# Kernel tuning notes

Hardware: AMD Instinct MI355X
Metric: run time of the kernel (lower is better)

## Reference

```python
import jax, jax.numpy as jnp
import numpy as np

D_MODEL = 2048
N_HEADS = 16
D_HEAD = 128
INIT_RANGE = 0.02
EPSILON = -100000.0  # mask fill value from the original module


def setup_inputs() -> dict:
    key = jax.random.key(0)
    ks = jax.random.split(key, 6)
    x = jax.random.normal(ks[0], (2, 2048, D_MODEL), dtype=jnp.float32)
    W_Q = jax.random.normal(ks[1], (N_HEADS, D_MODEL, D_HEAD), dtype=jnp.float32) * INIT_RANGE
    W_K = jax.random.normal(ks[2], (N_HEADS, D_MODEL, D_HEAD), dtype=jnp.float32) * INIT_RANGE
    W_V = jax.random.normal(ks[3], (N_HEADS, D_MODEL, D_HEAD), dtype=jnp.float32) * INIT_RANGE
    W_O = jax.random.normal(ks[4], (N_HEADS, D_HEAD, D_MODEL), dtype=jnp.float32) * INIT_RANGE
    b_Q = jnp.zeros((N_HEADS, D_HEAD), dtype=jnp.float32)
    b_K = jnp.zeros((N_HEADS, D_HEAD), dtype=jnp.float32)
    b_V = jnp.zeros((N_HEADS, D_HEAD), dtype=jnp.float32)
    b_O = jnp.zeros((D_MODEL,), dtype=jnp.float32)
    return {"normalized_resid_pre": x, "W_Q": W_Q, "b_Q": b_Q, "W_K": W_K,
            "b_K": b_K, "W_V": W_V, "b_V": b_V, "W_O": W_O, "b_O": b_O}


def reference(normalized_resid_pre, W_Q, b_Q, W_K, b_K, W_V, b_V, W_O, b_O):
    x = normalized_resid_pre  # [b, s, d_model]
    # per-head projections: [b, s, h, d_head]
    q = jnp.einsum('bsd,hdk->bshk', x, W_Q) + b_Q
    k = jnp.einsum('bsd,hdk->bshk', x, W_K) + b_K
    v = jnp.einsum('bsd,hdk->bshk', x, W_V) + b_V
    # attention scores [b, h, q, k]
    scores = jnp.einsum('bqhk,bshk->bhqs', q, k) / jnp.sqrt(jnp.float32(D_HEAD))
    S = scores.shape[-1]
    causal = jnp.tril(jnp.ones((S, S), dtype=bool))  # True = keep
    scores = jnp.where(causal, scores, jnp.float32(EPSILON))
    pattern = jax.nn.softmax(scores, axis=-1)
    z = jnp.einsum('bhqs,bshk->bqhk', pattern, v)
    attn_out = jnp.einsum('bqhk,hkd->bqd', z, W_O) + b_O
    return attn_out
```

## Files before the change

### kernel.cpp

```cpp
#include <hip/hip_runtime.h>
#include <hip/hip_bf16.h>

typedef unsigned short bfu;
typedef short          bf16x8 __attribute__((ext_vector_type(8)));
typedef float          floatx4 __attribute__((ext_vector_type(4)));
typedef unsigned short bfu4 __attribute__((ext_vector_type(4)));
typedef unsigned int   u32x2 __attribute__((ext_vector_type(2)));

__device__ __forceinline__ bfu f2bf(float f) {
    __hip_bfloat16 h = __float2bfloat16(f);
    return __builtin_bit_cast(unsigned short, h);
}

__device__ __forceinline__ void glds16(const bfu* g, bfu* l) {
    __builtin_amdgcn_global_load_lds(
        (const __attribute__((address_space(1))) unsigned int*)g,
        (__attribute__((address_space(3))) unsigned int*)l, 16, 0, 0);
}

#define BATCH 2
#define SEQ   2048
#define DM    2048
#define NH    16
#define DKH   128
#define SCALE 0.08838834764831845f

__global__ __launch_bounds__(256)
void cvt_x(const float* __restrict__ x, bfu* __restrict__ xb, int n) {
    const int i = (blockIdx.x * 256 + threadIdx.x) * 4;
    if (i >= n) return;
    const float4 v = *(const float4*)(x + i);
    bfu4 p; p[0] = f2bf(v.x); p[1] = f2bf(v.y); p[2] = f2bf(v.z); p[3] = f2bf(v.w);
    *(bfu4*)(xb + i) = p;
}

__device__ __forceinline__ void t64(const float* __restrict__ src,
                                    bfu* __restrict__ dst,
                                    int C, int r0, int c0, float s,
                                    float (*tile)[65]) {
    const int t  = threadIdx.x;
    const int lr = t >> 4;
    const int lc = (t & 15) * 4;
    #pragma unroll
    for (int pp = 0; pp < 4; pp++) {
        const float4 v = *(const float4*)(src + (size_t)(r0 + pp*16 + lr) * C + c0 + lc);
        tile[pp*16 + lr][lc + 0] = v.x;
        tile[pp*16 + lr][lc + 1] = v.y;
        tile[pp*16 + lr][lc + 2] = v.z;
        tile[pp*16 + lr][lc + 3] = v.w;
    }
    __syncthreads();
    const int rc = t & 15;
    const int cb = t >> 4;
    #pragma unroll
    for (int pp = 0; pp < 4; pp++) {
        const int c = pp*16 + cb;
        bfu4 pk;
        #pragma unroll
        for (int j = 0; j < 4; j++) pk[j] = f2bf(tile[rc*4 + j][c] * s);
        *(bfu4*)(dst + (size_t)(c0 + c) * DM + r0 + rc*4) = pk;
    }
}

__global__ __launch_bounds__(256)
void tcvt_qkv64(const float* __restrict__ WQ, const float* __restrict__ WK,
                const float* __restrict__ WV,
                bfu* __restrict__ WtQ, bfu* __restrict__ WtK, bfu* __restrict__ WtV) {
    __shared__ float tile[64][65];
    const int z = blockIdx.z;
    const int p = z >> 4, h = z & 15;
    const float* src = ((p == 0) ? WQ : (p == 1) ? WK : WV) + (size_t)h * DM * DKH;
    bfu*         dst = ((p == 0) ? WtQ : (p == 1) ? WtK : WtV) + (size_t)h * DKH * DM;
    const float  s   = (p == 0) ? SCALE : 1.0f;
    t64(src, dst, DKH, blockIdx.y * 64, blockIdx.x * 64, s, tile);
}

__global__ __launch_bounds__(256)
void tcvt_wo64(const float* __restrict__ WO, bfu* __restrict__ WtO) {
    __shared__ float tile[64][65];
    t64(WO, WtO, DM, blockIdx.y * 64, blockIdx.x * 64, 1.0f, tile);
}

__device__ __forceinline__ void stg_half(const bfu* gbase, bfu* slot,
                                         int wave, int lane, int csw) {
    #pragma unroll
    for (int l = 0; l < 2; l++) {
        const int j = l * 8 + wave;
        glds16(gbase + (size_t)((j >> 1) * 16 + (lane >> 2)) * DM
                     + (j & 1) * 32 + csw,
               slot + j * 512);
    }
}

__device__ __forceinline__ void ld_b8(bf16x8 (&bv)[4][2], const bfu* slot, int rdo) {
    #pragma unroll
    for (int n = 0; n < 4; n++)
        #pragma unroll
        for (int ks = 0; ks < 2; ks++)
            bv[n][ks] = *(const bf16x8*)&slot[(n * 2 + ks) * 512 + rdo];
}

__device__ __forceinline__ void ld_a8(bf16x8 (&af)[4][2], const bfu* slot, int rdo) {
    #pragma unroll
    for (int m = 0; m < 4; m++)
        #pragma unroll
        for (int ks = 0; ks < 2; ks++)
            af[m][ks] = *(const bf16x8*)&slot[(m * 2 + ks) * 512 + rdo];
}

template<int MH, int NHALF>
__device__ __forceinline__ void mfma16(floatx4 (&acc)[8][4],
                                       const bf16x8 (&af)[4][2],
                                       const bf16x8 (&bv)[4][2]) {
    __builtin_amdgcn_s_setprio(1);
    #pragma unroll
    for (int m = 0; m < 4; m++)
        #pragma unroll
        for (int n = 0; n < 2; n++)
            #pragma unroll
            for (int ks = 0; ks < 2; ks++)
                acc[MH*4 + m][NHALF*2 + n] =
                    __builtin_amdgcn_mfma_f32_16x16x32_bf16(
                        af[m][ks], bv[NHALF*2 + n][ks],
                        acc[MH*4 + m][NHALF*2 + n], 0, 0, 0);
    __builtin_amdgcn_s_setprio(0);
}

#define BARW()                                                      \
    __builtin_amdgcn_s_barrier();                                   \
    asm volatile("s_waitcnt lgkmcnt(0)" ::: "memory");              \
    __builtin_amdgcn_sched_barrier(0)

__global__ __launch_bounds__(512, 2)
void proj_qk8(const bfu* __restrict__ xb,
              const bfu* __restrict__ WtQ, const bfu* __restrict__ WtK,
              const float* __restrict__ bQ, const float* __restrict__ bK,
              bfu* __restrict__ Qall, bfu* __restrict__ Kall) {
    __shared__ __align__(16) bfu As[2][2][8192];
    __shared__ __align__(16) bfu Bs[2][2][8192];

    const int p = blockIdx.y >> 3;
    const bfu*   Wt   = (p == 0) ? WtQ : WtK;
    const float* bias = (p == 0) ? bQ  : bK;
    const float  bscale = (p == 0) ? SCALE : 1.0f;

    const int tid  = threadIdx.x;
    const int lane = tid & 63;
    const int wave = tid >> 6;
    const int lrow = lane & 15;
    const int quad = lane >> 4;
    const int wr   = wave >> 2;
    const int wc   = wave & 3;
    const size_t m0 = (size_t)blockIdx.x * 256;
    const int    n0 = (int)(blockIdx.y & 7) * 256;

    const int csw = ((lane & 3) * 8) ^ ((lane & 32) ? 16 : 0);
    const int rdo = lrow * 32 + ((quad * 8) ^ ((lrow & 8) ? 16 : 0));

    const bfu* Ab = xb + m0 * DM;
    const bfu* Bb = Wt + (size_t)n0 * DM;

    floatx4 acc[8][4] = {};
    bf16x8 af[4][2], bv[4][2];

#define STAGE_A(tau, h)                                                     \
    if ((tau) < 32) stg_half(Ab + (size_t)((h) * 128) * DM + (tau) * 64,    \
                             &As[(tau) & 1][h][0], wave, lane, csw)
#define STAGE_B(tau, h)                                                     \
    if ((tau) < 32) stg_half(Bb + (size_t)((h) * 128) * DM + (tau) * 64,    \
                             &Bs[(tau) & 1][h][0], wave, lane, csw)

    STAGE_B(0, 0); STAGE_B(0, 1); STAGE_A(0, 0); STAGE_A(0, 1);
    STAGE_B(1, 0); STAGE_B(1, 1); STAGE_A(1, 0);
    asm volatile("s_waitcnt vmcnt(6)" ::: "memory");
    __builtin_amdgcn_s_barrier();

    #pragma unroll 1
    for (int i = 0; i < 16; i++) {
        const int t0 = 2 * i;
        ld_b8(bv, &Bs[0][wc >> 1][(wc & 1) * 4096], rdo);
        ld_a8(af, &As[0][wr][0], rdo);
        STAGE_A(t0 + 1, 1);
        BARW();
        mfma16<0, 0>(acc, af, bv);
        __builtin_amdgcn_s_barrier();
        STAGE_B(t0 + 2, 0);
        BARW();
        mfma16<0, 1>(acc, af, bv);
        __builtin_amdgcn_s_barrier();
        ld_a8(af, &As[0][wr][4096], rdo);
        STAGE_B(t0 + 2, 1);
        BARW();
        mfma16<1, 0>(acc, af, bv);
        __builtin_amdgcn_s_barrier();
        STAGE_A(t0 + 2, 0);
        BARW();
        mfma16<1, 1>(acc, af, bv);
        if (i == 15) asm volatile("s_waitcnt vmcnt(0)" ::: "memory");
        else         asm volatile("s_waitcnt vmcnt(6)" ::: "memory");
        __builtin_amdgcn_s_barrier();
        ld_b8(bv, &Bs[1][wc >> 1][(wc & 1) * 4096], rdo);
        ld_a8(af, &As[1][wr][0], rdo);
        STAGE_A(t0 + 2, 1);
        BARW();
        mfma16<0, 0>(acc, af, bv);
        __builtin_amdgcn_s_barrier();
        STAGE_B(t0 + 3, 0);
        BARW();
        mfma16<0, 1>(acc, af, bv);
        __builtin_amdgcn_s_barrier();
        ld_a8(af, &As[1][wr][4096], rdo);
        STAGE_B(t0 + 3, 1);
        BARW();
        mfma16<1, 0>(acc, af, bv);
        __builtin_amdgcn_s_barrier();
        STAGE_A(t0 + 3, 0);
        BARW();
        mfma16<1, 1>(acc, af, bv);
        if (i < 15) asm volatile("s_waitcnt vmcnt(6)" ::: "memory");
        __builtin_amdgcn_s_barrier();
    }
#undef STAGE_A
#undef STAGE_B

    bfu* Out = (p == 0) ? Qall : Kall;
    #pragma unroll
    for (int m = 0; m < 8; m++) {
        #pragma unroll
        for (int n = 0; n < 4; n++) {
            const int gn = n0 + wc * 64 + n * 16 + lrow;
            const float bvv = bias[gn] * bscale;
            #pragma unroll
            for (int r = 0; r < 4; r++) {
                const size_t gm = m0 + wr * 128 + m * 16 + quad * 4 + r;
                Out[gm * DM + gn] = f2bf(acc[m][n][r] + bvv);
            }
        }
    }
}

__global__ __launch_bounds__(256)
void proj_v(const bfu* __restrict__ xb, const bfu* __restrict__ WtV,
            const float* __restrict__ bV, bfu* __restrict__ Vt) {
    __shared__ bfu As[128 * 32];
    __shared__ bfu Bs[128 * 32];
    const int tid  = threadIdx.x;
    const int lane = tid & 63;
    const int wave = tid >> 6;
    const int lrow = lane & 15;
    const int quad = lane >> 4;
    const int mw = (wave & 1) * 64;
    const int nw = (wave >> 1) * 64;
    const size_t m0 = (size_t)blockIdx.x * 128;
    const size_t n0 = (size_t)blockIdx.y * 128;
    const int rowb = lane >> 2;
    const int colb = (lane & 3) * 8;

    floatx4 acc[4][4] = {};

    for (int k0 = 0; k0 < DM; k0 += 32) {
        __syncthreads();
        #pragma unroll
        for (int i = 0; i < 2; i++) {
            const int rg = wave * 2 + i;
            glds16(xb  + (m0 + rg*16 + rowb) * DM + k0 + colb, &As[rg * 512]);
            glds16(WtV + (n0 + rg*16 + rowb) * DM + k0 + colb, &Bs[rg * 512]);
        }
        __syncthreads();
        bf16x8 af[4], bfr[4];
        #pragma unroll
        for (int t = 0; t < 4; t++) {
            af[t]  = *(const bf16x8*)&As[(mw + t*16 + lrow) * 32 + quad * 8];
            bfr[t] = *(const bf16x8*)&Bs[(nw + t*16 + lrow) * 32 + quad * 8];
        }
        #pragma unroll
        for (int mt = 0; mt < 4; mt++)
            #pragma unroll
            for (int nt = 0; nt < 4; nt++)
                acc[mt][nt] = __builtin_amdgcn_mfma_f32_16x16x32_bf16(
                                  af[mt], bfr[nt], acc[mt][nt], 0, 0, 0);
    }

    #pragma unroll
    for (int mt = 0; mt < 4; mt++) {
        #pragma unroll
        for (int nt = 0; nt < 4; nt++) {
            const int nl = (int)n0 + nw + nt*16 + lrow;
            const float bvv = bV[nl];
            const size_t gm0 = m0 + mw + mt*16 + quad*4;
            const int b = (int)(gm0 >> 11), s = (int)(gm0 & 2047);
            bfu4 pk;
            #pragma unroll
            for (int r = 0; r < 4; r++) pk[r] = f2bf(acc[mt][nt][r] + bvv);
            *(bfu4*)&Vt[((size_t)(b * NH + (nl >> 7)) * DKH + (nl & 127)) * SEQ + s] = pk;
        }
    }
}

__global__ __launch_bounds__(256)
void flash_attn(const bfu* __restrict__ Q, const bfu* __restrict__ K,
                const bfu* __restrict__ Vt, bfu* __restrict__ Z) {
    __shared__ bfu Ks[4][64][32];
    __shared__ bfu Vs[2][128][32];
    __shared__ bfu Ps[4][16][72];

    const int tid  = threadIdx.x;
    const int lane = tid & 63;
    const int wave = tid >> 6;
    const int lrow = lane & 15;
    const int quad = lane >> 4;
    const int hb = blockIdx.x;
    const int h = hb & 15, b = hb >> 4;
    const int qt = 31 - blockIdx.y;
    const int q0w = qt * 64 + wave * 16;
    const int rowb = lane >> 2;
    const int csw  = ((lane & 3) * 8) ^ ((lane & 32) ? 16 : 0);
    const int xr   = (lrow & 8) ? 16 : 0;
    const int rq0  = (quad * 8) ^ xr;

    const bfu* Qrow = Q + (size_t)(b * SEQ + q0w + lrow) * DM + h * DKH;
    bf16x8 qf[4];
    #pragma unroll
    for (int kc = 0; kc < 4; kc++)
        qf[kc] = *(const bf16x8*)(Qrow + kc*32 + quad*8);

    floatx4 z[8] = {};
    float l_loc = 0.f;
    const int qg = q0w + lrow;

    const bfu* Kb = K + (size_t)b * SEQ * DM + h * DKH;
    const bfu* Vb = Vt + (size_t)(b * NH + h) * DKH * SEQ;
    const int ntiles = qt + 1;

    for (int it = 0; it < ntiles; it++) {
        const int s0 = it * 64;
        __syncthreads();
        #pragma unroll
        for (int i = 0; i < 8; i++) {
            const int chunk = wave * 8 + i;
            if (chunk < 16) {
                const int kc = chunk >> 2, kg = chunk & 3;
                glds16(Kb + (size_t)(s0 + kg*16 + rowb) * DM + kc*32 + csw,
                       &Ks[kc][kg*16][0]);
            } else {
                const int c2 = chunk - 16;
                const int sh = c2 >> 3, dg = c2 & 7;
                glds16(Vb + (size_t)(dg*16 + rowb) * SEQ + s0 + sh*32 + csw,
                       &Vs[sh][dg*16][0]);
            }
        }
        __syncthreads();

        floatx4 sc[4];
        #pragma unroll
        for (int st = 0; st < 4; st++) {
            floatx4 a = {};
            #pragma unroll
            for (int kc = 0; kc < 4; kc++) {
                bf16x8 kf = *(const bf16x8*)&Ks[kc][st*16 + lrow][rq0];
                a = __builtin_amdgcn_mfma_f32_16x16x32_bf16(kf, qf[kc], a, 0, 0, 0);
            }
            sc[st] = a;
        }

        #pragma unroll
        for (int st = 0; st < 4; st++) {
            const int sbase = s0 + st*16 + quad*4;
            const float p0 = (sbase + 0 <= qg) ? __expf(sc[st][0]) : 0.f;
            const float p1 = (sbase + 1 <= qg) ? __expf(sc[st][1]) : 0.f;
            const float p2 = (sbase + 2 <= qg) ? __expf(sc[st][2]) : 0.f;
            const float p3 = (sbase + 3 <= qg) ? __expf(sc[st][3]) : 0.f;
            l_loc += (p0 + p1) + (p2 + p3);
            u32x2 pk;
            pk[0] = (unsigned)f2bf(p0) | ((unsigned)f2bf(p1) << 16);
            pk[1] = (unsigned)f2bf(p2) | ((unsigned)f2bf(p3) << 16);
            *(u32x2*)&Ps[wave][lrow][st*16 + quad*4] = pk;
        }

        bf16x8 pf0 = *(const bf16x8*)&Ps[wave][lrow][quad*8];
        bf16x8 pf1 = *(const bf16x8*)&Ps[wave][lrow][32 + quad*8];
        #pragma unroll
        for (int dt = 0; dt < 8; dt++) {
            bf16x8 v0 = *(const bf16x8*)&Vs[0][dt*16 + lrow][rq0];
            z[dt] = __builtin_amdgcn_mfma_f32_16x16x32_bf16(pf0, v0, z[dt], 0, 0, 0);
            bf16x8 v1 = *(const bf16x8*)&Vs[1][dt*16 + lrow][rq0];
            z[dt] = __builtin_amdgcn_mfma_f32_16x16x32_bf16(pf1, v1, z[dt], 0, 0, 0);
        }
    }

    float L = l_loc;
    L += __shfl_xor(L, 16);
    L += __shfl_xor(L, 32);
    float inv[4];
    #pragma unroll
    for (int r = 0; r < 4; r++)
        inv[r] = 1.0f / __shfl(L, quad*4 + r, 64);
    #pragma unroll
    for (int dt = 0; dt < 8; dt++) {
        #pragma unroll
        for (int r = 0; r < 4; r++) {
            const int qq = q0w + quad*4 + r;
            const int dk = dt*16 + lrow;
            Z[(size_t)(b * SEQ + qq) * DM + h * DKH + dk] = f2bf(z[dt][r] * inv[r]);
        }
    }
}

__global__ __launch_bounds__(256)
void out_gemm(const bfu* __restrict__ Zb, const bfu* __restrict__ WtO,
              const float* __restrict__ bO, float* out) {
    __shared__ bfu As[128 * 32];
    __shared__ bfu Bs[128 * 32];
    const int tid  = threadIdx.x;
    const int lane = tid & 63;
    const int wave = tid >> 6;
    const int lrow = lane & 15;
    const int quad = lane >> 4;
    const int mw = (wave & 1) * 64;
    const int nw = (wave >> 1) * 64;
    const size_t m0 = (size_t)blockIdx.x * 128;
    const size_t n0 = (size_t)blockIdx.y * 128;
    const int rowb = lane >> 2, colb = (lane & 3) * 8;

    floatx4 acc[4][4] = {};

    for (int k0 = 0; k0 < DM; k0 += 32) {
        __syncthreads();
        #pragma unroll
        for (int i = 0; i < 2; i++) {
            const int rg = wave * 2 + i;
            glds16(Zb  + (m0 + rg*16 + rowb) * DM + k0 + colb, &As[rg * 512]);
            glds16(WtO + (n0 + rg*16 + rowb) * DM + k0 + colb, &Bs[rg * 512]);
        }
        __syncthreads();
        bf16x8 af[4], bfr[4];
        #pragma unroll
        for (int t = 0; t < 4; t++) {
            af[t]  = *(const bf16x8*)&As[(mw + t*16 + lrow) * 32 + quad * 8];
            bfr[t] = *(const bf16x8*)&Bs[(nw + t*16 + lrow) * 32 + quad * 8];
        }
        #pragma unroll
        for (int mt = 0; mt < 4; mt++)
            #pragma unroll
            for (int nt = 0; nt < 4; nt++)
                acc[mt][nt] = __builtin_amdgcn_mfma_f32_16x16x32_bf16(
                                  af[mt], bfr[nt], acc[mt][nt], 0, 0, 0);
    }

    #pragma unroll
    for (int mt = 0; mt < 4; mt++) {
        #pragma unroll
        for (int nt = 0; nt < 4; nt++) {
            const size_t gn = n0 + nw + nt*16 + lrow;
            const float bv = bO[gn];
            #pragma unroll
            for (int r = 0; r < 4; r++) {
                const size_t gm = m0 + mw + mt*16 + quad*4 + r;
                out[gm * DM + gn] = acc[mt][nt][r] + bv;
            }
        }
    }
}

extern "C" void kernel_launch(void* const* d_in, const int* in_sizes, int n_in,
                              void* d_out, int out_size, void* d_ws, size_t ws_size,
                              hipStream_t stream) {
    const float* x  = (const float*)d_in[0];
    const float* WQ = (const float*)d_in[1];
    const float* bQ = (const float*)d_in[2];
    const float* WK = (const float*)d_in[3];
    const float* bK = (const float*)d_in[4];
    const float* WV = (const float*)d_in[5];
    const float* bV = (const float*)d_in[6];
    const float* WO = (const float*)d_in[7];
    const float* bO = (const float*)d_in[8];
    float* out = (float*)d_out;
    bfu* ws  = (bfu*)d_ws;
    bfu* dob = (bfu*)d_out;

    bfu* Qall = ws;
    bfu* Kall = Qall + 8388608;
    bfu* Vt   = Kall + 8388608;
    bfu* Zb   = Vt   + 8388608;
    bfu* WtV  = Zb;
    bfu* xb   = dob;
    bfu* WtQ  = dob + 8388608;
    bfu* WtK  = dob + 12582912;

    cvt_x<<<8192, 256, 0, stream>>>(x, xb, BATCH * SEQ * DM);

    tcvt_qkv64<<<dim3(2, 32, 48), 256, 0, stream>>>(WQ, WK, WV, WtQ, WtK, WtV);

    proj_qk8<<<dim3(16, 16), 512, 0, stream>>>(xb, WtQ, WtK, bQ, bK, Qall, Kall);
    proj_v<<<dim3(32, 16), 256, 0, stream>>>(xb, WtV, bV, Vt);

    flash_attn<<<dim3(32, 32), 256, 0, stream>>>(Qall, Kall, Vt, Zb);

    tcvt_wo64<<<dim3(32, 32), 256, 0, stream>>>(WO, Qall);
    out_gemm<<<dim3(32, 16), 256, 0, stream>>>(Zb, Qall, bO, out);
}
```

Baseline: 362.0 us.

## Process 32 query rows per wave in flash attention to reuse K/V tiles

Each wave now handles two 16-row query blocks (128 queries per workgroup instead of 64), so every K and V tile loaded into shared memory feeds twice as many MFMAs. Grid size is halved in the query dimension and the P staging buffer is doubled. This cuts global-to-LDS traffic and barrier count per unit of work, at the cost of more registers per thread (launch bounds hint of 3 blocks per CU), fewer workgroups, and coarser causal load imbalance.

New measurement: 383.8 us. 6.0% more time.

```diff
diff --git a/kernel.cpp b/kernel.cpp
--- a/kernel.cpp
+++ b/kernel.cpp
@@ -297,12 +297,12 @@
     }
 }
 
-__global__ __launch_bounds__(256)
+__global__ __launch_bounds__(256, 3)
 void flash_attn(const bfu* __restrict__ Q, const bfu* __restrict__ K,
                 const bfu* __restrict__ Vt, bfu* __restrict__ Z) {
     __shared__ bfu Ks[4][64][32];
     __shared__ bfu Vs[2][128][32];
-    __shared__ bfu Ps[4][16][72];
+    __shared__ bfu Ps[4][32][72];
 
     const int tid  = threadIdx.x;
     const int lane = tid & 63;
@@ -311,26 +311,29 @@
     const int quad = lane >> 4;
     const int hb = blockIdx.x;
     const int h = hb & 15, b = hb >> 4;
-    const int qt = 31 - blockIdx.y;
-    const int q0w = qt * 64 + wave * 16;
+    const int qt = 15 - blockIdx.y;
+    const int q0w = qt * 128 + wave * 32;
     const int rowb = lane >> 2;
     const int csw  = ((lane & 3) * 8) ^ ((lane & 32) ? 16 : 0);
-    const int xr   = (lrow & 8) ? 16 : 0;
-    const int rq0  = (quad * 8) ^ xr;
-
-    const bfu* Qrow = Q + (size_t)(b * SEQ + q0w + lrow) * DM + h * DKH;
-    bf16x8 qf[4];
-    #pragma unroll
-    for (int kc = 0; kc < 4; kc++)
-        qf[kc] = *(const bf16x8*)(Qrow + kc*32 + quad*8);
-
-    floatx4 z[8] = {};
-    float l_loc = 0.f;
-    const int qg = q0w + lrow;
+    const int rq0  = (quad * 8) ^ ((lrow & 8) ? 16 : 0);
+
+    const bfu* Qrow0 = Q + (size_t)(b * SEQ + q0w + lrow) * DM + h * DKH;
+    const bfu* Qrow1 = Qrow0 + (size_t)16 * DM;
+    bf16x8 qf0[4], qf1[4];
+    #pragma unroll
+    for (int kc = 0; kc < 4; kc++) {
+        qf0[kc] = *(const bf16x8*)(Qrow0 + kc*32 + quad*8);
+        qf1[kc] = *(const bf16x8*)(Qrow1 + kc*32 + quad*8);
+    }
+
+    floatx4 z0[8] = {}, z1[8] = {};
+    float l0 = 0.f, l1 = 0.f;
+    const int qg0 = q0w + lrow;
+    const int qg1 = q0w + 16 + lrow;
 
     const bfu* Kb = K + (size_t)b * SEQ * DM + h * DKH;
     const bfu* Vb = Vt + (size_t)(b * NH + h) * DKH * SEQ;
-    const int ntiles = qt + 1;
+    const int ntiles = 2 * (qt + 1);
 
     for (int it = 0; it < ntiles; it++) {
         const int s0 = it * 64;
@@ -351,57 +354,73 @@
         }
         __syncthreads();
 
-        floatx4 sc[4];
         #pragma unroll
         for (int st = 0; st < 4; st++) {
-            floatx4 a = {};
+            floatx4 a0 = {}, a1 = {};
             #pragma unroll
             for (int kc = 0; kc < 4; kc++) {
                 bf16x8 kf = *(const bf16x8*)&Ks[kc][st*16 + lrow][rq0];
-                a = __builtin_amdgcn_mfma_f32_16x16x32_bf16(kf, qf[kc], a, 0, 0, 0);
+                a0 = __builtin_amdgcn_mfma_f32_16x16x32_bf16(kf, qf0[kc], a0, 0, 0, 0);
+                a1 = __builtin_amdgcn_mfma_f32_16x16x32_bf16(kf, qf1[kc], a1, 0, 0, 0);
             }
-            sc[st] = a;
-        }
-
-        #pragma unroll
-        for (int st = 0; st < 4; st++) {
             const int sbase = s0 + st*16 + quad*4;
-            const float p0 = (sbase + 0 <= qg) ? __expf(sc[st][0]) : 0.f;
-            const float p1 = (sbase + 1 <= qg) ? __expf(sc[st][1]) : 0.f;
-            const float p2 = (sbase + 2 <= qg) ? __expf(sc[st][2]) : 0.f;
-            const float p3 = (sbase + 3 <= qg) ? __expf(sc[st][3]) : 0.f;
-            l_loc += (p0 + p1) + (p2 + p3);
-            u32x2 pk;
-            pk[0] = (unsigned)f2bf(p0) | ((unsigned)f2bf(p1) << 16);
-            pk[1] = (unsigned)f2bf(p2) | ((unsigned)f2bf(p3) << 16);
-            *(u32x2*)&Ps[wave][lrow][st*16 + quad*4] = pk;
-        }
-
-        bf16x8 pf0 = *(const bf16x8*)&Ps[wave][lrow][quad*8];
-        bf16x8 pf1 = *(const bf16x8*)&Ps[wave][lrow][32 + quad*8];
+            {
+                const float p0 = (sbase + 0 <= qg0) ? __expf(a0[0]) : 0.f;
+                const float p1 = (sbase + 1 <= qg0) ? __expf(a0[1]) : 0.f;
+                const float p2 = (sbase + 2 <= qg0) ? __expf(a0[2]) : 0.f;
+                const float p3 = (sbase + 3 <= qg0) ? __expf(a0[3]) : 0.f;
+                l0 += (p0 + p1) + (p2 + p3);
+                u32x2 pk;
+                pk[0] = (unsigned)f2bf(p0) | ((unsigned)f2bf(p1) << 16);
+                pk[1] = (unsigned)f2bf(p2) | ((unsigned)f2bf(p3) << 16);
+                *(u32x2*)&Ps[wave][lrow][st*16 + quad*4] = pk;
+            }
+            {
+                const float p0 = (sbase + 0 <= qg1) ? __expf(a1[0]) : 0.f;
+                const float p1 = (sbase + 1 <= qg1) ? __expf(a1[1]) : 0.f;
+                const float p2 = (sbase + 2 <= qg1) ? __expf(a1[2]) : 0.f;
+                const float p3 = (sbase + 3 <= qg1) ? __expf(a1[3]) : 0.f;
+                l1 += (p0 + p1) + (p2 + p3);
+                u32x2 pk;
+                pk[0] = (unsigned)f2bf(p0) | ((unsigned)f2bf(p1) << 16);
+                pk[1] = (unsigned)f2bf(p2) | ((unsigned)f2bf(p3) << 16);
+                *(u32x2*)&Ps[wave][16 + lrow][st*16 + quad*4] = pk;
+            }
+        }
+
+        bf16x8 pf00 = *(const bf16x8*)&Ps[wave][lrow][quad*8];
+        bf16x8 pf01 = *(const bf16x8*)&Ps[wave][lrow][32 + quad*8];
+        bf16x8 pf10 = *(const bf16x8*)&Ps[wave][16 + lrow][quad*8];
+        bf16x8 pf11 = *(const bf16x8*)&Ps[wave][16 + lrow][32 + quad*8];
         #pragma unroll
         for (int dt = 0; dt < 8; dt++) {
             bf16x8 v0 = *(const bf16x8*)&Vs[0][dt*16 + lrow][rq0];
-            z[dt] = __builtin_amdgcn_mfma_f32_16x16x32_bf16(pf0, v0, z[dt], 0, 0, 0);
+            z0[dt] = __builtin_amdgcn_mfma_f32_16x16x32_bf16(pf00, v0, z0[dt], 0, 0, 0);
+            z1[dt] = __builtin_amdgcn_mfma_f32_16x16x32_bf16(pf10, v0, z1[dt], 0, 0, 0);
             bf16x8 v1 = *(const bf16x8*)&Vs[1][dt*16 + lrow][rq0];
-            z[dt] = __builtin_amdgcn_mfma_f32_16x16x32_bf16(pf1, v1, z[dt], 0, 0, 0);
-        }
-    }
-
-    float L = l_loc;
-    L += __shfl_xor(L, 16);
-    L += __shfl_xor(L, 32);
-    float inv[4];
-    #pragma unroll
-    for (int r = 0; r < 4; r++)
-        inv[r] = 1.0f / __shfl(L, quad*4 + r, 64);
+            z0[dt] = __builtin_amdgcn_mfma_f32_16x16x32_bf16(pf01, v1, z0[dt], 0, 0, 0);
+            z1[dt] = __builtin_amdgcn_mfma_f32_16x16x32_bf16(pf11, v1, z1[dt], 0, 0, 0);
+        }
+    }
+
+    float L0 = l0, L1 = l1;
+    L0 += __shfl_xor(L0, 16);  L0 += __shfl_xor(L0, 32);
+    L1 += __shfl_xor(L1, 16);  L1 += __shfl_xor(L1, 32);
+    float inv0[4], inv1[4];
+    #pragma unroll
+    for (int r = 0; r < 4; r++) {
+        inv0[r] = 1.0f / __shfl(L0, quad*4 + r, 64);
+        inv1[r] = 1.0f / __shfl(L1, quad*4 + r, 64);
+    }
     #pragma unroll
     for (int dt = 0; dt < 8; dt++) {
         #pragma unroll
         for (int r = 0; r < 4; r++) {
-            const int qq = q0w + quad*4 + r;
             const int dk = dt*16 + lrow;
-            Z[(size_t)(b * SEQ + qq) * DM + h * DKH + dk] = f2bf(z[dt][r] * inv[r]);
+            const int qq0 = q0w + quad*4 + r;
+            Z[(size_t)(b * SEQ + qq0) * DM + h * DKH + dk] = f2bf(z0[dt][r] * inv0[r]);
+            const int qq1 = q0w + 16 + quad*4 + r;
+            Z[(size_t)(b * SEQ + qq1) * DM + h * DKH + dk] = f2bf(z1[dt][r] * inv1[r]);
         }
     }
 }
@@ -494,7 +513,7 @@
     proj_qk8<<<dim3(16, 16), 512, 0, stream>>>(xb, WtQ, WtK, bQ, bK, Qall, Kall);
     proj_v<<<dim3(32, 16), 256, 0, stream>>>(xb, WtV, bV, Vt);
 
-    flash_attn<<<dim3(32, 32), 256, 0, stream>>>(Qall, Kall, Vt, Zb);
+    flash_attn<<<dim3(32, 16), 256, 0, stream>>>(Qall, Kall, Vt, Zb);
 
     tcvt_wo64<<<dim3(32, 32), 256, 0, stream>>>(WO, Qall);
     out_gemm<<<dim3(32, 16), 256, 0, stream>>>(Zb, Qall, bO, out);
```
